# Kernel optimization log

Measured on AMD Instinct MI355X. Metric: run time of the kernel, lower is better.

The kernel has to match this reference:

```python
import jax, jax.numpy as jnp
import numpy as np

MAX_DEPTH = 6
NUM_TREES = 64
LEAF_DIMS = 128
D_IN = 512
BATCH = 4096
N_INTERNAL = 2 ** MAX_DEPTH - 1  # 63
N_LEAVES = 2 ** MAX_DEPTH        # 64


def setup_inputs() -> dict:
    key = jax.random.key(0)
    ks = jax.random.split(key, 4)
    x = jax.random.normal(ks[0], (BATCH, D_IN), dtype=jnp.float32)
    # Stacked internal-node dense layers, node i at index i (level order, node_index ordering)
    W = jax.random.normal(ks[1], (N_INTERNAL, D_IN, NUM_TREES), dtype=jnp.float32) / np.sqrt(D_IN)
    b = jnp.zeros((N_INTERNAL, NUM_TREES), dtype=jnp.float32)
    leaf_weight = jax.random.normal(ks[2], (N_LEAVES, LEAF_DIMS, NUM_TREES), dtype=jnp.float32)
    gates = jax.random.normal(ks[3], (N_LEAVES, LEAF_DIMS, NUM_TREES), dtype=jnp.float32)
    return {"x": x, "W": W, "b": b, "leaf_weight": leaf_weight, "gates": gates}


def reference(x, W, b, leaf_weight, gates):
    # All internal-node gating probabilities in one batched matmul:
    # g[b, n, t] = sigmoid(x[b] @ W[n] + b[n])  for every internal node n, tree t
    g = jax.nn.sigmoid(jnp.einsum('bd,ndt->bnt', x, W) + b[None, :, :])  # [B, 63, T]

    B = x.shape[0]
    T = W.shape[-1]
    # Path probability to each leaf, built level by level.
    # Level l has 2^l nodes at internal indices [2^l - 1, 2^(l+1) - 2];
    # interleaving (left=p*g, right=p*(1-g)) matches node_index child ordering.
    p = jnp.ones((B, 1, T), dtype=x.dtype)
    for level in range(MAX_DEPTH):
        start = 2 ** level - 1
        n_lvl = 2 ** level
        gl = g[:, start:start + n_lvl, :]                  # [B, n_lvl, T]
        children = jnp.stack([p * gl, p * (1.0 - gl)], axis=2)  # [B, n_lvl, 2, T]
        p = children.reshape(B, 2 * n_lvl, T)
    # p: [B, n_leaves, T] leaf path probabilities

    # Softmax mixture-of-experts gate over trees, then weighted leaf mixture:
    # out[b, d] = sum_{l, t} p[b, l, t] * leaf_weight[l, d, t] * softmax(gates, -1)[l, d, t]
    w = leaf_weight * jax.nn.softmax(gates, axis=-1)  # [L, D, T]
    out = jnp.einsum('blt,ldt->bd', p, w)
    return out
```

## Files before the change

### kernel.cpp

```cpp
#include <hip/hip_runtime.h>
#include <stdint.h>

#define BATCH 4096
#define DIN   512
#define NT    64
#define NL    64
#define LD    128

typedef __attribute__((ext_vector_type(8))) short bf16x8;
typedef __attribute__((ext_vector_type(8))) _Float16 f16x8;
typedef __attribute__((ext_vector_type(4))) float f32x4;

typedef const __attribute__((address_space(1))) unsigned char* gcp_t;
typedef __attribute__((address_space(3))) unsigned char* lp_t;

__device__ __forceinline__ void gl_lds16(const void* g, void* l) {
  __builtin_amdgcn_global_load_lds((gcp_t)g, (lp_t)l, 16, 0, 0);
}

__device__ __forceinline__ unsigned pk_bf16(float a, float b) {
  union { float f; unsigned u; } ua, ub;
  ua.f = a; ub.f = b;
  return __builtin_amdgcn_perm(ub.u + 0x8000u, ua.u + 0x8000u, 0x07060302u);
}

__device__ __forceinline__ unsigned short f2bf(float f) {
  union { float f; unsigned u; } a; a.f = f;
  return (unsigned short)((a.u + 0x8000u) >> 16);
}

__global__ __launch_bounds__(256) void prep_all_k(
    const float* __restrict__ x, const float* __restrict__ W,
    const float* __restrict__ gates, const float* __restrict__ lw,
    unsigned short* __restrict__ xb, unsigned short* __restrict__ Wt,
    unsigned short* __restrict__ Wv2) {
  __shared__ float smem[12288];
  const int bx = blockIdx.x;
  const int tid = threadIdx.x;

  if (bx < 2048) {
    int i = bx * 256 + tid;
    float4 v = ((const float4*)x)[i];
    uint2 o;
    o.x = pk_bf16(v.x, v.y);
    o.y = pk_bf16(v.z, v.w);
    ((uint2*)xb)[i] = o;
  } else if (bx < 2304) {
    int bb = bx - 2048;
    int n = bb >> 2, d0 = (bb & 3) * 128;
    float* buf = smem;
    if (n < 63) {
      for (int it = 0; it < 32; ++it) {
        int idx = it * 256 + tid;
        buf[idx] = W[n * 32768 + (d0 + (idx >> 6)) * 64 + (idx & 63)];
      }
    }
    __syncthreads();
    int t = tid >> 2, q = tid & 3;
    unsigned vals[16];
    #pragma unroll
    for (int j = 0; j < 16; ++j) {
      float va = (n < 63) ? buf[(q * 32 + 2 * j) * 64 + t] : 0.0f;
      float vb = (n < 63) ? buf[(q * 32 + 2 * j + 1) * 64 + t] : 0.0f;
      vals[j] = (n < 63) ? pk_bf16(va, vb) : 0u;
    }
    uint4* dst = (uint4*)(Wt + t * 32768 + n * 512 + d0 + q * 32);
    const uint4* src = (const uint4*)vals;
    dst[0] = src[0]; dst[1] = src[1]; dst[2] = src[2]; dst[3] = src[3];
  } else {
    int d = bx - 2304;
    float* gb = smem;
    float* lb = smem + 4096;
    float* wv = smem + 8192;
    for (int it = 0; it < 16; ++it) {
      int idx = it * 256 + tid;
      int l = idx >> 6;
      int ga = l * 8192 + d * 64 + (idx & 63);
      gb[idx] = gates[ga];
      lb[idx] = lw[ga];
    }
    __syncthreads();
    int wave = tid >> 6, lane = tid & 63;
    for (int l = wave; l < 64; l += 4) {
      float v = gb[l * 64 + lane];
      float mx = v;
      for (int m = 32; m >= 1; m >>= 1) mx = fmaxf(mx, __shfl_xor(mx, m));
      float e = __expf(v - mx);
      float s = e;
      for (int m = 32; m >= 1; m >>= 1) s += __shfl_xor(s, m);
      wv[l * 64 + lane] = lb[l * 64 + lane] * e / s;
    }
    __syncthreads();
    #pragma unroll
    for (int c = 0; c < 2; ++c) {
      int k0 = tid * 16 + c * 8;
      unsigned o[4];
      #pragma unroll
      for (int j = 0; j < 4; ++j) {
        int ka = k0 + 2 * j, kb = k0 + 2 * j + 1;
        o[j] = pk_bf16(wv[(ka & 63) * 64 + (ka >> 6)], wv[(kb & 63) * 64 + (kb >> 6)]);
      }
      *(uint4*)(Wv2 + (long)d * 4096 + k0) = *(const uint4*)o;
    }
  }
}

__global__ __launch_bounds__(256, 4) void gemm1_tree_k(
    const unsigned short* __restrict__ xb,
    const unsigned short* __restrict__ Wt,
    const float* __restrict__ bias,
    unsigned short* __restrict__ P)
{
  __shared__ __align__(16) char smem[34816];
  __shared__ float bb[128];
  unsigned short* AsB = (unsigned short*)smem;
  unsigned short* BsB = (unsigned short*)(smem + 16384);
  _Float16* gbuf = (_Float16*)smem;

  const int tid = threadIdx.x;
  const int wave = tid >> 6, lane = tid & 63;
  const int b0 = blockIdx.x * 128;
  const int t0 = blockIdx.y * 2;

  if (tid < 128) {
    int n = tid & 63, t = t0 + (tid >> 6);
    bb[tid] = (n < 63) ? bias[n * 64 + t] : 0.0f;
  }

  const f32x4 zero = {0.f, 0.f, 0.f, 0.f};
  f32x4 acc[4][4];
  #pragma unroll
  for (int i = 0; i < 4; ++i)
    #pragma unroll
    for (int j = 0; j < 4; ++j) acc[i][j] = zero;

  const int g0 = wave * 64 + lane;
  const int g1 = g0 + 256;
  const int c0 = ((g0 & 3) ^ ((g0 >> 3) & 3)) * 8;
  const int c1 = ((g1 & 3) ^ ((g1 >> 3) & 3)) * 8;
  const unsigned short* Ag0 = xb + (long)(b0 + (g0 >> 2)) * 512 + c0;
  const unsigned short* Ag1 = xb + (long)(b0 + (g1 >> 2)) * 512 + c1;
  const unsigned short* Bg0 = Wt + (long)(t0 * 64 + (g0 >> 2)) * 512 + c0;
  const unsigned short* Bg1 = Wt + (long)(t0 * 64 + (g1 >> 2)) * 512 + c1;
  const int lofs0 = wave * 512;
  const int lofs1 = wave * 512 + 2048;

  const int wm = (wave >> 1) * 64, wn = (wave & 1) * 64;
  const int mrow = lane & 15, kg = lane >> 4;
  const int slot = (kg ^ ((mrow >> 1) & 3)) * 8;

  gl_lds16(Ag0, AsB + lofs0);
  gl_lds16(Ag1, AsB + lofs1);
  gl_lds16(Bg0, BsB + lofs0);
  gl_lds16(Bg1, BsB + lofs1);

  for (int it = 0; it < 16; ++it) {
    const int buf = (it & 1) * 4096;
    if (it < 15) {
      const int kk = (it + 1) * 32;
      const int nbuf = ((it + 1) & 1) * 4096;
      gl_lds16(Ag0 + kk, AsB + nbuf + lofs0);
      gl_lds16(Ag1 + kk, AsB + nbuf + lofs1);
      gl_lds16(Bg0 + kk, BsB + nbuf + lofs0);
      gl_lds16(Bg1 + kk, BsB + nbuf + lofs1);
      asm volatile("s_waitcnt vmcnt(4)" ::: "memory");
    } else {
      asm volatile("s_waitcnt vmcnt(0)" ::: "memory");
    }
    asm volatile("s_barrier" ::: "memory");

    bf16x8 fa[4], fb[4];
    #pragma unroll
    for (int i = 0; i < 4; ++i)
      fa[i] = *(const bf16x8*)(AsB + buf + (wm + i * 16 + mrow) * 32 + slot);
    #pragma unroll
    for (int j = 0; j < 4; ++j)
      fb[j] = *(const bf16x8*)(BsB + buf + (wn + j * 16 + mrow) * 32 + slot);
    #pragma unroll
    for (int i = 0; i < 4; ++i)
      #pragma unroll
      for (int j = 0; j < 4; ++j)
        acc[i][j] = __builtin_amdgcn_mfma_f32_16x16x32_bf16(fa[i], fb[j], acc[i][j], 0, 0, 0);

    asm volatile("s_waitcnt lgkmcnt(0)" ::: "memory");
    asm volatile("s_barrier" ::: "memory");
  }

  #pragma unroll
  for (int i = 0; i < 4; ++i)
    #pragma unroll
    for (int j = 0; j < 4; ++j) {
      int col = wn + j * 16 + mrow;
      float bv = bb[col];
      #pragma unroll
      for (int r = 0; r < 4; ++r) {
        int row = wm + i * 16 + kg * 4 + r;
        float z = acc[i][j][r] + bv;
        gbuf[row * 136 + col] = (_Float16)__builtin_amdgcn_rcpf(1.0f + __expf(-z));
      }
    }
  __syncthreads();

  {
    const int row = tid >> 1, tr = tid & 1;
    const _Float16* grow = gbuf + row * 136 + tr * 64;
    float g[63];
    #pragma unroll
    for (int c = 0; c < 8; ++c) {
      f16x8 gv = *(const f16x8*)(grow + c * 8);
      #pragma unroll
      for (int j = 0; j < 8; ++j) {
        int n = c * 8 + j;
        if (n < 63) g[n] = (float)gv[j];
      }
    }
    float P3[8];
    {
      float a0 = g[0],            a1 = 1.0f - g[0];
      float c0_ = a0 * g[1],      c1_ = a0 * (1.0f - g[1]);
      float c2_ = a1 * g[2],      c3_ = a1 * (1.0f - g[2]);
      P3[0] = c0_ * g[3];  P3[1] = c0_ * (1.0f - g[3]);
      P3[2] = c1_ * g[4];  P3[3] = c1_ * (1.0f - g[4]);
      P3[4] = c2_ * g[5];  P3[5] = c2_ * (1.0f - g[5]);
      P3[6] = c3_ * g[6];  P3[7] = c3_ * (1.0f - g[6]);
    }
    unsigned short* prow = P + (long)(b0 + row) * 4096 + (t0 + tr) * 64;
    #pragma unroll
    for (int o = 0; o < 8; ++o) {
      float g3 = g[7 + o];
      float q0 = P3[o] * g3, q1 = P3[o] * (1.0f - g3);
      float g4a = g[15 + 2 * o], g4b = g[16 + 2 * o];
      float r0 = q0 * g4a, r1 = q0 * (1.0f - g4a);
      float r2 = q1 * g4b, r3 = q1 * (1.0f - g4b);
      unsigned ou[4];
      #pragma unroll
      for (int h = 0; h < 4; ++h) {
        float g5 = g[31 + 4 * o + h];
        float rr = (h == 0) ? r0 : (h == 1) ? r1 : (h == 2) ? r2 : r3;
        ou[h] = pk_bf16(rr * g5, rr * (1.0f - g5));
      }
      *(uint4*)(prow + o * 8) = *(const uint4*)ou;
    }
  }
}

__global__ __launch_bounds__(256, 4) void gemm2_k(
    const unsigned short* __restrict__ P,
    const unsigned short* __restrict__ Wv2,
    float* __restrict__ out)
{
  __shared__ unsigned short AsB[2][64 * 32];
  __shared__ unsigned short BsB[2][128 * 32];
  const int tid = threadIdx.x;
  const int wave = tid >> 6, lane = tid & 63;
  const int b0 = blockIdx.x * 64;
  const int k0 = blockIdx.y * 1024;

  const f32x4 zero = {0.f, 0.f, 0.f, 0.f};
  f32x4 acc[2][4];
  #pragma unroll
  for (int i = 0; i < 2; ++i)
    #pragma unroll
    for (int j = 0; j < 4; ++j) acc[i][j] = zero;

  const int g0 = wave * 64 + lane;
  const int g1 = g0 + 256;
  const int c0 = ((g0 & 3) ^ ((g0 >> 3) & 3)) * 8;
  const int c1 = ((g1 & 3) ^ ((g1 >> 3) & 3)) * 8;
  const unsigned short* Ag0 = P + (long)(b0 + (g0 >> 2)) * 4096 + k0 + c0;
  const unsigned short* Bg0 = Wv2 + (long)(g0 >> 2) * 4096 + k0 + c0;
  const unsigned short* Bg1 = Wv2 + (long)(g1 >> 2) * 4096 + k0 + c1;
  const int lofs = wave * 512;

  const int wm = (wave >> 1) * 32, wn = (wave & 1) * 64;
  const int mrow = lane & 15, kg = lane >> 4;
  const int slot = (kg ^ ((mrow >> 1) & 3)) * 8;

  gl_lds16(Ag0, AsB[0] + lofs);
  gl_lds16(Bg0, BsB[0] + lofs);
  gl_lds16(Bg1, BsB[0] + lofs + 2048);

  for (int it = 0; it < 32; ++it) {
    const int buf = it & 1;
    if (it < 31) {
      const int kk = (it + 1) * 32;
      const int nbuf = (it + 1) & 1;
      gl_lds16(Ag0 + kk, AsB[nbuf] + lofs);
      gl_lds16(Bg0 + kk, BsB[nbuf] + lofs);
      gl_lds16(Bg1 + kk, BsB[nbuf] + lofs + 2048);
      asm volatile("s_waitcnt vmcnt(3)" ::: "memory");
    } else {
      asm volatile("s_waitcnt vmcnt(0)" ::: "memory");
    }
    asm volatile("s_barrier" ::: "memory");

    bf16x8 fa[2], fb[4];
    #pragma unroll
    for (int i = 0; i < 2; ++i)
      fa[i] = *(const bf16x8*)(AsB[buf] + (wm + i * 16 + mrow) * 32 + slot);
    #pragma unroll
    for (int j = 0; j < 4; ++j)
      fb[j] = *(const bf16x8*)(BsB[buf] + (wn + j * 16 + mrow) * 32 + slot);
    #pragma unroll
    for (int i = 0; i < 2; ++i)
      #pragma unroll
      for (int j = 0; j < 4; ++j)
        acc[i][j] = __builtin_amdgcn_mfma_f32_16x16x32_bf16(fa[i], fb[j], acc[i][j], 0, 0, 0);

    asm volatile("s_waitcnt lgkmcnt(0)" ::: "memory");
    asm volatile("s_barrier" ::: "memory");
  }

  #pragma unroll
  for (int i = 0; i < 2; ++i)
    #pragma unroll
    for (int j = 0; j < 4; ++j) {
      int col = wn + j * 16 + mrow;
      #pragma unroll
      for (int r = 0; r < 4; ++r) {
        int row = wm + i * 16 + kg * 4 + r;
        atomicAdd(&out[(long)(b0 + row) * 128 + col], acc[i][j][r]);
      }
    }
}

extern "C" void kernel_launch(void* const* d_in, const int* in_sizes, int n_in,
                              void* d_out, int out_size, void* d_ws, size_t ws_size,
                              hipStream_t stream) {
  const float* x     = (const float*)d_in[0];
  const float* W     = (const float*)d_in[1];
  const float* b     = (const float*)d_in[2];
  const float* lw    = (const float*)d_in[3];
  const float* gates = (const float*)d_in[4];
  float* out = (float*)d_out;

  char* ws = (char*)d_ws;
  unsigned short* xb  = (unsigned short*)(ws);
  unsigned short* Wt  = (unsigned short*)(ws + (4l  << 20));
  unsigned short* Wv2 = (unsigned short*)(ws + (8l  << 20));
  unsigned short* P   = (unsigned short*)(ws + (16l << 20));

  hipMemsetAsync(out, 0, (size_t)4096 * 128 * sizeof(float), stream);
  hipLaunchKernelGGL(prep_all_k,   dim3(2432),   dim3(256), 0, stream,
                     x, W, gates, lw, xb, Wt, Wv2);
  hipLaunchKernelGGL(gemm1_tree_k, dim3(32, 32), dim3(256), 0, stream, xb, Wt, b, P);
  hipLaunchKernelGGL(gemm2_k,      dim3(64, 4),  dim3(256), 0, stream, P, Wv2, out);
}
```

Measured before the change: 137.8 us.

## Triple-buffer both GEMM LDS pipelines, drop a barrier, and split-K gemm2 further

Both GEMM kernels move from double to triple buffering of the LDS tiles, prefetching two K-steps ahead. This lets each iteration use a single barrier placed before the next prefetch instead of two. gemm2 also halves its K chunk per block and doubles the grid to 512 blocks, giving more parallelism at the cost of twice the atomicAdd traffic into the output. gemm1's larger LDS footprint lowers its occupancy hint from 4 to 3 blocks per CU.

```diff
diff --git a/kernel.cpp b/kernel.cpp
--- a/kernel.cpp
+++ b/kernel.cpp
@@ -105,16 +105,16 @@
   }
 }
 
-__global__ __launch_bounds__(256, 4) void gemm1_tree_k(
+__global__ __launch_bounds__(256, 3) void gemm1_tree_k(
     const unsigned short* __restrict__ xb,
     const unsigned short* __restrict__ Wt,
     const float* __restrict__ bias,
     unsigned short* __restrict__ P)
 {
-  __shared__ __align__(16) char smem[34816];
+  __shared__ __align__(16) char smem[49152];
   __shared__ float bb[128];
   unsigned short* AsB = (unsigned short*)smem;
-  unsigned short* BsB = (unsigned short*)(smem + 16384);
+  unsigned short* BsB = (unsigned short*)(smem + 24576);
   _Float16* gbuf = (_Float16*)smem;
 
   const int tid = threadIdx.x;
@@ -153,21 +153,28 @@
   gl_lds16(Ag1, AsB + lofs1);
   gl_lds16(Bg0, BsB + lofs0);
   gl_lds16(Bg1, BsB + lofs1);
-
+  gl_lds16(Ag0 + 32, AsB + 4096 + lofs0);
+  gl_lds16(Ag1 + 32, AsB + 4096 + lofs1);
+  gl_lds16(Bg0 + 32, BsB + 4096 + lofs0);
+  gl_lds16(Bg1 + 32, BsB + 4096 + lofs1);
+
+  #pragma unroll
   for (int it = 0; it < 16; ++it) {
-    const int buf = (it & 1) * 4096;
+    const int buf = (it % 3) * 4096;
     if (it < 15) {
-      const int kk = (it + 1) * 32;
-      const int nbuf = ((it + 1) & 1) * 4096;
+      asm volatile("s_waitcnt vmcnt(4) lgkmcnt(0)" ::: "memory");
+    } else {
+      asm volatile("s_waitcnt vmcnt(0) lgkmcnt(0)" ::: "memory");
+    }
+    asm volatile("s_barrier" ::: "memory");
+    if (it < 14) {
+      const int kk = (it + 2) * 32;
+      const int nbuf = ((it + 2) % 3) * 4096;
       gl_lds16(Ag0 + kk, AsB + nbuf + lofs0);
       gl_lds16(Ag1 + kk, AsB + nbuf + lofs1);
       gl_lds16(Bg0 + kk, BsB + nbuf + lofs0);
       gl_lds16(Bg1 + kk, BsB + nbuf + lofs1);
-      asm volatile("s_waitcnt vmcnt(4)" ::: "memory");
-    } else {
-      asm volatile("s_waitcnt vmcnt(0)" ::: "memory");
-    }
-    asm volatile("s_barrier" ::: "memory");
+    }
 
     bf16x8 fa[4], fb[4];
     #pragma unroll
@@ -181,10 +188,9 @@
       #pragma unroll
       for (int j = 0; j < 4; ++j)
         acc[i][j] = __builtin_amdgcn_mfma_f32_16x16x32_bf16(fa[i], fb[j], acc[i][j], 0, 0, 0);
-
-    asm volatile("s_waitcnt lgkmcnt(0)" ::: "memory");
-    asm volatile("s_barrier" ::: "memory");
-  }
+  }
+
+  __syncthreads();
 
   #pragma unroll
   for (int i = 0; i < 4; ++i)
@@ -249,12 +255,12 @@
     const unsigned short* __restrict__ Wv2,
     float* __restrict__ out)
 {
-  __shared__ unsigned short AsB[2][64 * 32];
-  __shared__ unsigned short BsB[2][128 * 32];
+  __shared__ unsigned short AsB[3][64 * 32];
+  __shared__ unsigned short BsB[3][128 * 32];
   const int tid = threadIdx.x;
   const int wave = tid >> 6, lane = tid & 63;
   const int b0 = blockIdx.x * 64;
-  const int k0 = blockIdx.y * 1024;
+  const int k0 = blockIdx.y * 512;
 
   const f32x4 zero = {0.f, 0.f, 0.f, 0.f};
   f32x4 acc[2][4];
@@ -279,20 +285,26 @@
   gl_lds16(Ag0, AsB[0] + lofs);
   gl_lds16(Bg0, BsB[0] + lofs);
   gl_lds16(Bg1, BsB[0] + lofs + 2048);
-
-  for (int it = 0; it < 32; ++it) {
-    const int buf = it & 1;
-    if (it < 31) {
-      const int kk = (it + 1) * 32;
-      const int nbuf = (it + 1) & 1;
+  gl_lds16(Ag0 + 32, AsB[1] + lofs);
+  gl_lds16(Bg0 + 32, BsB[1] + lofs);
+  gl_lds16(Bg1 + 32, BsB[1] + lofs + 2048);
+
+  #pragma unroll
+  for (int it = 0; it < 16; ++it) {
+    const int buf = it % 3;
+    if (it < 15) {
+      asm volatile("s_waitcnt vmcnt(3) lgkmcnt(0)" ::: "memory");
+    } else {
+      asm volatile("s_waitcnt vmcnt(0) lgkmcnt(0)" ::: "memory");
+    }
+    asm volatile("s_barrier" ::: "memory");
+    if (it < 14) {
+      const int kk = (it + 2) * 32;
+      const int nbuf = (it + 2) % 3;
       gl_lds16(Ag0 + kk, AsB[nbuf] + lofs);
       gl_lds16(Bg0 + kk, BsB[nbuf] + lofs);
       gl_lds16(Bg1 + kk, BsB[nbuf] + lofs + 2048);
-      asm volatile("s_waitcnt vmcnt(3)" ::: "memory");
-    } else {
-      asm volatile("s_waitcnt vmcnt(0)" ::: "memory");
-    }
-    asm volatile("s_barrier" ::: "memory");
+    }
 
     bf16x8 fa[2], fb[4];
     #pragma unroll
@@ -306,9 +318,6 @@
       #pragma unroll
       for (int j = 0; j < 4; ++j)
         acc[i][j] = __builtin_amdgcn_mfma_f32_16x16x32_bf16(fa[i], fb[j], acc[i][j], 0, 0, 0);
-
-    asm volatile("s_waitcnt lgkmcnt(0)" ::: "memory");
-    asm volatile("s_barrier" ::: "memory");
   }
 
   #pragma unroll
@@ -344,5 +353,5 @@
   hipLaunchKernelGGL(prep_all_k,   dim3(2432),   dim3(256), 0, stream,
                      x, W, gates, lw, xb, Wt, Wv2);
   hipLaunchKernelGGL(gemm1_tree_k, dim3(32, 32), dim3(256), 0, stream, xb, Wt, b, P);
-  hipLaunchKernelGGL(gemm2_k,      dim3(64, 4),  dim3(256), 0, stream, P, Wv2, out);
-}
+  hipLaunchKernelGGL(gemm2_k,      dim3(64, 8),  dim3(256), 0, stream, P, Wv2, out);
+}
```

New measurement: 141.7 us. +2.8%, slower.

## Fold output zeroing into prep kernel and shrink gemm1 LDS for occupancy

Applied to the files above, without the earlier changes.

Drops the separate hipMemsetAsync by adding 32 extra blocks to the prep kernel that zero the output buffer. In gemm1 the bias now goes into registers instead of a shared array, and the padded 136-stride gate buffer becomes a 128-stride XOR-swizzled layout. Together these cut LDS to 32KB so the launch bound can rise from 4 to 5 blocks per CU. The risks are register pressure under the tighter bound and whether the swizzle stays free of bank conflicts.

```diff
diff --git a/kernel.cpp b/kernel.cpp
--- a/kernel.cpp
+++ b/kernel.cpp
@@ -33,7 +33,7 @@
     const float* __restrict__ x, const float* __restrict__ W,
     const float* __restrict__ gates, const float* __restrict__ lw,
     unsigned short* __restrict__ xb, unsigned short* __restrict__ Wt,
-    unsigned short* __restrict__ Wv2) {
+    unsigned short* __restrict__ Wv2, float* __restrict__ out) {
   __shared__ float smem[12288];
   const int bx = blockIdx.x;
   const int tid = threadIdx.x;
@@ -67,7 +67,7 @@
     uint4* dst = (uint4*)(Wt + t * 32768 + n * 512 + d0 + q * 32);
     const uint4* src = (const uint4*)vals;
     dst[0] = src[0]; dst[1] = src[1]; dst[2] = src[2]; dst[3] = src[3];
-  } else {
+  } else if (bx < 2432) {
     int d = bx - 2304;
     float* gb = smem;
     float* lb = smem + 4096;
@@ -102,17 +102,23 @@
       }
       *(uint4*)(Wv2 + (long)d * 4096 + k0) = *(const uint4*)o;
     }
-  }
-}
-
-__global__ __launch_bounds__(256, 4) void gemm1_tree_k(
+  } else {
+    float4 z = {0.f, 0.f, 0.f, 0.f};
+    int base = (bx - 2432) * 256 + tid;
+    float4* o4 = (float4*)out;
+    #pragma unroll
+    for (int k = 0; k < 16; ++k)
+      o4[k * 8192 + base] = z;
+  }
+}
+
+__global__ __launch_bounds__(256, 5) void gemm1_tree_k(
     const unsigned short* __restrict__ xb,
     const unsigned short* __restrict__ Wt,
     const float* __restrict__ bias,
     unsigned short* __restrict__ P)
 {
-  __shared__ __align__(16) char smem[34816];
-  __shared__ float bb[128];
+  __shared__ __align__(16) char smem[32768];
   unsigned short* AsB = (unsigned short*)smem;
   unsigned short* BsB = (unsigned short*)(smem + 16384);
   _Float16* gbuf = (_Float16*)smem;
@@ -122,9 +128,15 @@
   const int b0 = blockIdx.x * 128;
   const int t0 = blockIdx.y * 2;
 
-  if (tid < 128) {
-    int n = tid & 63, t = t0 + (tid >> 6);
-    bb[tid] = (n < 63) ? bias[n * 64 + t] : 0.0f;
+  const int wm = (wave >> 1) * 64, wn = (wave & 1) * 64;
+  const int mrow = lane & 15, kg = lane >> 4;
+  const int slot = (kg ^ ((mrow >> 1) & 3)) * 8;
+
+  float bv[4];
+  #pragma unroll
+  for (int j = 0; j < 4; ++j) {
+    int n = j * 16 + mrow;
+    bv[j] = (n < 63) ? bias[n * 64 + t0 + (wave & 1)] : 0.0f;
   }
 
   const f32x4 zero = {0.f, 0.f, 0.f, 0.f};
@@ -144,10 +156,6 @@
   const unsigned short* Bg1 = Wt + (long)(t0 * 64 + (g1 >> 2)) * 512 + c1;
   const int lofs0 = wave * 512;
   const int lofs1 = wave * 512 + 2048;
-
-  const int wm = (wave >> 1) * 64, wn = (wave & 1) * 64;
-  const int mrow = lane & 15, kg = lane >> 4;
-  const int slot = (kg ^ ((mrow >> 1) & 3)) * 8;
 
   gl_lds16(Ag0, AsB + lofs0);
   gl_lds16(Ag1, AsB + lofs1);
@@ -191,23 +199,25 @@
     #pragma unroll
     for (int j = 0; j < 4; ++j) {
       int col = wn + j * 16 + mrow;
-      float bv = bb[col];
+      int oct = col >> 3, sub = col & 7;
       #pragma unroll
       for (int r = 0; r < 4; ++r) {
         int row = wm + i * 16 + kg * 4 + r;
-        float z = acc[i][j][r] + bv;
-        gbuf[row * 136 + col] = (_Float16)__builtin_amdgcn_rcpf(1.0f + __expf(-z));
+        float z = acc[i][j][r] + bv[j];
+        gbuf[row * 128 + ((oct ^ (row & 15)) << 3) + sub] =
+            (_Float16)__builtin_amdgcn_rcpf(1.0f + __expf(-z));
       }
     }
   __syncthreads();
 
   {
     const int row = tid >> 1, tr = tid & 1;
-    const _Float16* grow = gbuf + row * 136 + tr * 64;
+    const _Float16* grow = gbuf + row * 128;
+    const int rx = row & 15;
     float g[63];
     #pragma unroll
     for (int c = 0; c < 8; ++c) {
-      f16x8 gv = *(const f16x8*)(grow + c * 8);
+      f16x8 gv = *(const f16x8*)(grow + (((tr * 8 + c) ^ rx) << 3));
       #pragma unroll
       for (int j = 0; j < 8; ++j) {
         int n = c * 8 + j;
@@ -340,9 +350,8 @@
   unsigned short* Wv2 = (unsigned short*)(ws + (8l  << 20));
   unsigned short* P   = (unsigned short*)(ws + (16l << 20));
 
-  hipMemsetAsync(out, 0, (size_t)4096 * 128 * sizeof(float), stream);
-  hipLaunchKernelGGL(prep_all_k,   dim3(2432),   dim3(256), 0, stream,
-                     x, W, gates, lw, xb, Wt, Wv2);
+  hipLaunchKernelGGL(prep_all_k,   dim3(2464),   dim3(256), 0, stream,
+                     x, W, gates, lw, xb, Wt, Wv2, out);
   hipLaunchKernelGGL(gemm1_tree_k, dim3(32, 32), dim3(256), 0, stream, xb, Wt, b, P);
   hipLaunchKernelGGL(gemm2_k,      dim3(64, 4),  dim3(256), 0, stream, P, Wv2, out);
 }
```

After: 182.8 us. +32.6%, slower.
